# Kernel optimization log

Hardware: AMD Instinct MI355X
Metric: run time of the kernel (lower is better)

Reference implementation:

```python
import jax, jax.numpy as jnp
import numpy as np

T = 2048   # sequence length
K = 8      # anchor stride
B = 8      # batch
E = 64     # head dim


def make_coords(t, k):
    # Faithful vectorized version of get_coords2: for each anchor c in
    # {0, k, 2k, ...}, emit pairs (y, c) for y in [c, t).
    cs = np.arange(t // k) * k
    rows = np.concatenate([np.arange(c, t) for c in cs]).astype(np.int32)
    cols = np.concatenate([np.full(t - c, c, dtype=np.int32) for c in cs])
    return rows, cols


def setup_inputs() -> dict:
    key = jax.random.key(0)
    k1, k2, k3 = jax.random.split(key, 3)
    rows, cols = make_coords(T, K)  # np = 263168 nonzeros
    return {
        "k": jax.random.normal(k1, (B, T, E), dtype=jnp.float32),
        "q": jax.random.normal(k2, (B, T, E), dtype=jnp.float32),
        "v": jax.random.normal(k3, (B, T, E), dtype=jnp.float32),
        "rows": jnp.asarray(rows),
        "cols": jnp.asarray(cols),
    }


def reference(k, q, v, rows, cols):
    # dot[b, p] = <k[b, rows[p], :], q[b, cols[p], :]>  (calc_vals on k @ q^T)
    # out[b, y, :] = sum_{p: rows[p]==y} dot[b, p] * v[b, cols[p], :]
    #   (sparse.batchmm: sparse (t x t) matrix with values dot, times v)
    t = k.shape[1]

    def single(kb, qb, vb):
        dots = jnp.einsum("pe,pe->p", kb[rows], qb[cols])           # [np]
        contrib = dots[:, None] * vb[cols]                           # [np, e]
        return jax.ops.segment_sum(contrib, rows, num_segments=t)   # [t, e]

    return jax.vmap(single)(k, q, v)
```

## Files before the change

kernel.cpp:

```cpp
#include <hip/hip_runtime.h>
#include <hip/hip_bf16.h>


constexpr int T_LEN = 2048;
constexpr int EDIM  = 64;
constexpr int ROWS  = 32;
constexpr int NTILE = T_LEN / ROWS;
constexpr int TE    = T_LEN * EDIM;

typedef __attribute__((ext_vector_type(4))) float f32x4;
typedef __attribute__((ext_vector_type(8))) short bf16x8;

__device__ __forceinline__ short f2bf(float f) {
    __hip_bfloat16 h = __float2bfloat16(f);
    return __builtin_bit_cast(short, h);
}

__device__ __forceinline__ bf16x8 pack8(f32x4 a, f32x4 b) {
    bf16x8 r;
    r[0] = f2bf(a[0]); r[1] = f2bf(a[1]); r[2] = f2bf(a[2]); r[3] = f2bf(a[3]);
    r[4] = f2bf(b[0]); r[5] = f2bf(b[1]); r[6] = f2bf(b[2]); r[7] = f2bf(b[3]);
    return r;
}

__device__ __forceinline__ bf16x8 pack8a(const float* v) {
    bf16x8 r;
    #pragma unroll
    for (int i = 0; i < 8; ++i) r[i] = f2bf(v[i]);
    return r;
}

__device__ __forceinline__ void run_tile(const float* __restrict__ kb,
                                         const float* __restrict__ qb,
                                         const float* __restrict__ vb,
                                         int y0, int wpar, int lane,
                                         short* sl, f32x4 (&acc)[2][4])
{
    const int g  = lane >> 4;
    const int ln = lane & 15;

    bf16x8 Kf[2][2];
    #pragma unroll
    for (int mt = 0; mt < 2; ++mt)
        #pragma unroll
        for (int eh = 0; eh < 2; ++eh) {
            const float* p = kb + (size_t)(y0 + mt * 16 + ln) * EDIM + eh * 32 + g * 8;
            Kf[mt][eh] = pack8(*(const f32x4*)p, *(const f32x4*)(p + 4));
        }

    const int amax = (y0 + ROWS - 1) >> 3;
    const int nat  = (amax >> 5) + 1;

    for (int ai = wpar; ai < nat; ai += 2) {
        const int a0 = ai * 32;

        f32x4 qraw[2][2][2];
        #pragma unroll
        for (int nt = 0; nt < 2; ++nt)
            #pragma unroll
            for (int eh = 0; eh < 2; ++eh) {
                const float* p = qb + (size_t)(8 * (a0 + nt * 16 + ln)) * EDIM + eh * 32 + g * 8;
                qraw[nt][eh][0] = *(const f32x4*)p;
                qraw[nt][eh][1] = *(const f32x4*)(p + 4);
            }

        float vraw[4][8];
        {
            const float* pv = vb + (size_t)(8 * (a0 + 8 * g)) * EDIM + ln;
            #pragma unroll
            for (int i = 0; i < 8; ++i)
                #pragma unroll
                for (int et = 0; et < 4; ++et)
                    vraw[et][i] = pv[(size_t)i * 8 * EDIM + et * 16];
        }

        bf16x8 Qf[2][2];
        #pragma unroll
        for (int nt = 0; nt < 2; ++nt)
            #pragma unroll
            for (int eh = 0; eh < 2; ++eh)
                Qf[nt][eh] = pack8(qraw[nt][eh][0], qraw[nt][eh][1]);

        f32x4 S[2][2];
        #pragma unroll
        for (int mt = 0; mt < 2; ++mt)
            #pragma unroll
            for (int nt = 0; nt < 2; ++nt) {
                f32x4 s = {0.f, 0.f, 0.f, 0.f};
                s = __builtin_amdgcn_mfma_f32_16x16x32_bf16(Kf[mt][0], Qf[nt][0], s, 0, 0, 0);
                s = __builtin_amdgcn_mfma_f32_16x16x32_bf16(Kf[mt][1], Qf[nt][1], s, 0, 0, 0);
                S[mt][nt] = s;
            }

        if (ai == nat - 1) {
            #pragma unroll
            for (int mt = 0; mt < 2; ++mt)
                #pragma unroll
                for (int nt = 0; nt < 2; ++nt)
                    #pragma unroll
                    for (int r = 0; r < 4; ++r) {
                        int y = y0 + mt * 16 + g * 4 + r;
                        int a = a0 + nt * 16 + ln;
                        if (8 * a > y) S[mt][nt][r] = 0.f;
                    }
        }

        #pragma unroll
        for (int mt = 0; mt < 2; ++mt)
            #pragma unroll
            for (int nt = 0; nt < 2; ++nt)
                #pragma unroll
                for (int r = 0; r < 4; ++r) {
                    int row = mt * 16 + g * 4 + r;
                    int a   = nt * 16 + ln;
                    sl[row * 32 + (((a >> 3) ^ (row & 3)) << 3) + (a & 7)] = f2bf(S[mt][nt][r]);
                }

        bf16x8 SA[2];
        #pragma unroll
        for (int mt = 0; mt < 2; ++mt) {
            int row = mt * 16 + ln;
            SA[mt] = *(const bf16x8*)(sl + row * 32 + ((g ^ (row & 3)) << 3));
        }

        #pragma unroll
        for (int et = 0; et < 4; ++et) {
            bf16x8 Vf = pack8a(vraw[et]);
            #pragma unroll
            for (int mt = 0; mt < 2; ++mt)
                acc[mt][et] = __builtin_amdgcn_mfma_f32_16x16x32_bf16(SA[mt], Vf, acc[mt][et], 0, 0, 0);
        }
    }
}

__device__ __forceinline__ void write_partial(float (*pb)[EDIM], f32x4 (&acc)[2][4],
                                              int g, int ln)
{
    #pragma unroll
    for (int mt = 0; mt < 2; ++mt)
        #pragma unroll
        for (int et = 0; et < 4; ++et)
            #pragma unroll
            for (int r = 0; r < 4; ++r) {
                int row = mt * 16 + g * 4 + r;
                int e   = et * 16 + ln;
                pb[row][e ^ ((row & 3) << 2)] = acc[mt][et][r];
            }
}

__device__ __forceinline__ void store_add(float* o, float (*pb)[EDIM],
                                          f32x4 (&acc)[2][4], int g, int ln)
{
    #pragma unroll
    for (int mt = 0; mt < 2; ++mt)
        #pragma unroll
        for (int et = 0; et < 4; ++et)
            #pragma unroll
            for (int r = 0; r < 4; ++r) {
                int row = mt * 16 + g * 4 + r;
                int e   = et * 16 + ln;
                o[(size_t)row * EDIM + e] = acc[mt][et][r] + pb[row][e ^ ((row & 3) << 2)];
            }
}

__global__ __launch_bounds__(128, 1)
void sh2_mfma(const float* __restrict__ kk, const float* __restrict__ qq,
              const float* __restrict__ vv, float* __restrict__ out, int B)
{
    __shared__ alignas(16) short slds[2][ROWS * 32];
    __shared__ float pbuf[2][ROWS][EDIM];

    const int bid  = blockIdx.x;
    const int p    = bid & 31;
    const int b    = bid >> 5;
    const int w    = threadIdx.x >> 6;
    const int lane = threadIdx.x & 63;
    const int g = lane >> 4, ln = lane & 15;

    const float* kb = kk + (size_t)b * TE;
    const float* qb = qq + (size_t)b * TE;
    const float* vb = vv + (size_t)b * TE;

    const int y0A = ROWS * p;
    const int y0B = ROWS * (NTILE - 1 - p);

    const f32x4 vzero = {0.f, 0.f, 0.f, 0.f};
    f32x4 accA[2][4], accB[2][4];
    #pragma unroll
    for (int i = 0; i < 2; ++i)
        #pragma unroll
        for (int j = 0; j < 4; ++j) { accA[i][j] = vzero; accB[i][j] = vzero; }

    run_tile(kb, qb, vb, y0A, w, lane, slds[w], accA);
    if (w == 1) write_partial(pbuf[0], accA, g, ln);

    run_tile(kb, qb, vb, y0B, w, lane, slds[w], accB);
    if (w == 0) write_partial(pbuf[1], accB, g, ln);

    __syncthreads();

    if (w == 0) store_add(out + (size_t)b * TE + (size_t)y0A * EDIM, pbuf[0], accA, g, ln);
    else        store_add(out + (size_t)b * TE + (size_t)y0B * EDIM, pbuf[1], accB, g, ln);
}

extern "C" void kernel_launch(void* const* d_in, const int* in_sizes, int n_in,
                              void* d_out, int out_size, void* d_ws, size_t ws_size,
                              hipStream_t stream) {
    const float* kk = (const float*)d_in[0];
    const float* qq = (const float*)d_in[1];
    const float* vv = (const float*)d_in[2];
    float* o        = (float*)d_out;
    int B = in_sizes[0] / TE;
    sh2_mfma<<<B * (NTILE / 2), 128, 0, stream>>>(kk, qq, vv, o, B);
}
```

Baseline: 12.41 us.

## Precompute bf16 K, anchor Q and transposed V in a prep kernel

Adds a prep kernel that converts K to bf16, gathers the anchor rows of Q into a compact bf16 array, and writes V anchors transposed in bf16 to the workspace. The main kernel then loads MFMA operands directly as bf16x8 vectors instead of doing strided fp32 loads and per-element conversion. Work is redistributed to one 32-row tile per block with four waves splitting the anchor loop, reduced through padded shared memory. This costs a second launch and an extra global round trip through the workspace, and removes the tile pairing that balanced the triangular work per block.

```diff
diff --git a/kernel.cpp b/kernel.cpp
--- a/kernel.cpp
+++ b/kernel.cpp
@@ -4,89 +4,116 @@
 
 constexpr int T_LEN = 2048;
 constexpr int EDIM  = 64;
+constexpr int NA    = 256;
 constexpr int ROWS  = 32;
 constexpr int NTILE = T_LEN / ROWS;
 constexpr int TE    = T_LEN * EDIM;
+constexpr int AE    = NA * EDIM;
 
 typedef __attribute__((ext_vector_type(4))) float f32x4;
 typedef __attribute__((ext_vector_type(8))) short bf16x8;
+typedef __attribute__((ext_vector_type(4))) short bf16x4;
 
 __device__ __forceinline__ short f2bf(float f) {
     __hip_bfloat16 h = __float2bfloat16(f);
     return __builtin_bit_cast(short, h);
 }
 
-__device__ __forceinline__ bf16x8 pack8(f32x4 a, f32x4 b) {
-    bf16x8 r;
-    r[0] = f2bf(a[0]); r[1] = f2bf(a[1]); r[2] = f2bf(a[2]); r[3] = f2bf(a[3]);
-    r[4] = f2bf(b[0]); r[5] = f2bf(b[1]); r[6] = f2bf(b[2]); r[7] = f2bf(b[3]);
-    return r;
+__global__ __launch_bounds__(256)
+void sh2_prep(const float* __restrict__ kk, const float* __restrict__ qq,
+              const float* __restrict__ vv, short* __restrict__ ws, int B)
+{
+    const int nK = B * TE / 4;
+    const int nQ = B * AE / 4;
+    short* Qa = ws;
+    short* Vt = ws + (size_t)B * AE;
+    short* Kb = ws + (size_t)2 * B * AE;
+
+    int tid = blockIdx.x * 256 + threadIdx.x;
+    if (tid < nK) {
+        f32x4 x = *(const f32x4*)(kk + (size_t)tid * 4);
+        bf16x4 r;
+        #pragma unroll
+        for (int i = 0; i < 4; ++i) r[i] = f2bf(x[i]);
+        *(bf16x4*)(Kb + (size_t)tid * 4) = r;
+    } else if (tid < nK + nQ) {
+        int t = tid - nK;
+        int e4 = t & 15, a = (t >> 4) & 255, b = t >> 12;
+        f32x4 x = *(const f32x4*)(qq + ((size_t)b * T_LEN + 8 * a) * EDIM + e4 * 4);
+        bf16x4 r;
+        #pragma unroll
+        for (int i = 0; i < 4; ++i) r[i] = f2bf(x[i]);
+        *(bf16x4*)(Qa + (size_t)t * 4) = r;
+    } else if (tid < nK + 2 * nQ) {
+        int t = tid - nK - nQ;
+        int a4 = t & 63, e = (t >> 6) & 63, b = t >> 12;
+        bf16x4 r;
+        #pragma unroll
+        for (int i = 0; i < 4; ++i)
+            r[i] = f2bf(vv[((size_t)b * T_LEN + 8 * (a4 * 4 + i)) * EDIM + e]);
+        *(bf16x4*)(Vt + (size_t)t * 4) = r;
+    }
 }
 
-__device__ __forceinline__ bf16x8 pack8a(const float* v) {
-    bf16x8 r;
-    #pragma unroll
-    for (int i = 0; i < 8; ++i) r[i] = f2bf(v[i]);
-    return r;
-}
+constexpr int EP = 76;
 
-__device__ __forceinline__ void run_tile(const float* __restrict__ kb,
-                                         const float* __restrict__ qb,
-                                         const float* __restrict__ vb,
-                                         int y0, int wpar, int lane,
-                                         short* sl, f32x4 (&acc)[2][4])
+__global__ __launch_bounds__(256, 2)
+void sh2_main(const short* __restrict__ ws, float* __restrict__ out, int B)
 {
-    const int g  = lane >> 4;
-    const int ln = lane & 15;
+    __shared__ alignas(16) short slds[4][ROWS * 32];
+    __shared__ float pbuf[4][ROWS][EP];
+
+    const int bid = blockIdx.x;
+    const int p   = NTILE - 1 - (bid >> 3);
+    const int b   = bid & 7;
+    const int w    = threadIdx.x >> 6;
+    const int lane = threadIdx.x & 63;
+    const int g = lane >> 4, ln = lane & 15;
+
+    const short* Qa = ws + (size_t)b * AE;
+    const short* Vt = ws + (size_t)B * AE + (size_t)b * AE;
+    const short* Kb = ws + (size_t)2 * B * AE + (size_t)b * TE;
+
+    const int y0  = ROWS * p;
+    const int nat = (((4 * p + 3) >> 5)) + 1;
 
     bf16x8 Kf[2][2];
     #pragma unroll
     for (int mt = 0; mt < 2; ++mt)
         #pragma unroll
-        for (int eh = 0; eh < 2; ++eh) {
-            const float* p = kb + (size_t)(y0 + mt * 16 + ln) * EDIM + eh * 32 + g * 8;
-            Kf[mt][eh] = pack8(*(const f32x4*)p, *(const f32x4*)(p + 4));
-        }
+        for (int eh = 0; eh < 2; ++eh)
+            Kf[mt][eh] = *(const bf16x8*)(Kb + (size_t)(y0 + mt * 16 + ln) * EDIM + eh * 32 + g * 8);
 
-    const int amax = (y0 + ROWS - 1) >> 3;
-    const int nat  = (amax >> 5) + 1;
+    const f32x4 vzero = {0.f, 0.f, 0.f, 0.f};
+    f32x4 acc[2][4];
+    #pragma unroll
+    for (int i = 0; i < 2; ++i)
+        #pragma unroll
+        for (int j = 0; j < 4; ++j) acc[i][j] = vzero;
 
-    for (int ai = wpar; ai < nat; ai += 2) {
+    short* sl = slds[w];
+
+    for (int ai = w; ai < nat; ai += 4) {
         const int a0 = ai * 32;
-
-        f32x4 qraw[2][2][2];
-        #pragma unroll
-        for (int nt = 0; nt < 2; ++nt)
-            #pragma unroll
-            for (int eh = 0; eh < 2; ++eh) {
-                const float* p = qb + (size_t)(8 * (a0 + nt * 16 + ln)) * EDIM + eh * 32 + g * 8;
-                qraw[nt][eh][0] = *(const f32x4*)p;
-                qraw[nt][eh][1] = *(const f32x4*)(p + 4);
-            }
-
-        float vraw[4][8];
-        {
-            const float* pv = vb + (size_t)(8 * (a0 + 8 * g)) * EDIM + ln;
-            #pragma unroll
-            for (int i = 0; i < 8; ++i)
-                #pragma unroll
-                for (int et = 0; et < 4; ++et)
-                    vraw[et][i] = pv[(size_t)i * 8 * EDIM + et * 16];
-        }
 
         bf16x8 Qf[2][2];
         #pragma unroll
         for (int nt = 0; nt < 2; ++nt)
             #pragma unroll
             for (int eh = 0; eh < 2; ++eh)
-                Qf[nt][eh] = pack8(qraw[nt][eh][0], qraw[nt][eh][1]);
+                Qf[nt][eh] = *(const bf16x8*)(Qa + (size_t)(a0 + nt * 16 + ln) * EDIM + eh * 32 + g * 8);
+
+        bf16x8 Vf[4];
+        #pragma unroll
+        for (int et = 0; et < 4; ++et)
+            Vf[et] = *(const bf16x8*)(Vt + (size_t)(et * 16 + ln) * NA + a0 + g * 8);
 
         f32x4 S[2][2];
         #pragma unroll
         for (int mt = 0; mt < 2; ++mt)
             #pragma unroll
             for (int nt = 0; nt < 2; ++nt) {
-                f32x4 s = {0.f, 0.f, 0.f, 0.f};
+                f32x4 s = vzero;
                 s = __builtin_amdgcn_mfma_f32_16x16x32_bf16(Kf[mt][0], Qf[nt][0], s, 0, 0, 0);
                 s = __builtin_amdgcn_mfma_f32_16x16x32_bf16(Kf[mt][1], Qf[nt][1], s, 0, 0, 0);
                 S[mt][nt] = s;
@@ -113,94 +140,44 @@
                 for (int r = 0; r < 4; ++r) {
                     int row = mt * 16 + g * 4 + r;
                     int a   = nt * 16 + ln;
-                    sl[row * 32 + (((a >> 3) ^ (row & 3)) << 3) + (a & 7)] = f2bf(S[mt][nt][r]);
+                    sl[row * 32 + ((((a >> 3) ^ ((row >> 2) & 3))) << 3) + (a & 7)] = f2bf(S[mt][nt][r]);
                 }
 
         bf16x8 SA[2];
         #pragma unroll
         for (int mt = 0; mt < 2; ++mt) {
             int row = mt * 16 + ln;
-            SA[mt] = *(const bf16x8*)(sl + row * 32 + ((g ^ (row & 3)) << 3));
+            SA[mt] = *(const bf16x8*)(sl + row * 32 + ((g ^ ((row >> 2) & 3)) << 3));
         }
 
         #pragma unroll
-        for (int et = 0; et < 4; ++et) {
-            bf16x8 Vf = pack8a(vraw[et]);
+        for (int et = 0; et < 4; ++et)
             #pragma unroll
             for (int mt = 0; mt < 2; ++mt)
-                acc[mt][et] = __builtin_amdgcn_mfma_f32_16x16x32_bf16(SA[mt], Vf, acc[mt][et], 0, 0, 0);
-        }
+                acc[mt][et] = __builtin_amdgcn_mfma_f32_16x16x32_bf16(SA[mt], Vf[et], acc[mt][et], 0, 0, 0);
     }
-}
 
-__device__ __forceinline__ void write_partial(float (*pb)[EDIM], f32x4 (&acc)[2][4],
-                                              int g, int ln)
-{
     #pragma unroll
     for (int mt = 0; mt < 2; ++mt)
         #pragma unroll
         for (int et = 0; et < 4; ++et)
             #pragma unroll
-            for (int r = 0; r < 4; ++r) {
-                int row = mt * 16 + g * 4 + r;
-                int e   = et * 16 + ln;
-                pb[row][e ^ ((row & 3) << 2)] = acc[mt][et][r];
-            }
-}
-
-__device__ __forceinline__ void store_add(float* o, float (*pb)[EDIM],
-                                          f32x4 (&acc)[2][4], int g, int ln)
-{
-    #pragma unroll
-    for (int mt = 0; mt < 2; ++mt)
-        #pragma unroll
-        for (int et = 0; et < 4; ++et)
-            #pragma unroll
-            for (int r = 0; r < 4; ++r) {
-                int row = mt * 16 + g * 4 + r;
-                int e   = et * 16 + ln;
-                o[(size_t)row * EDIM + e] = acc[mt][et][r] + pb[row][e ^ ((row & 3) << 2)];
-            }
-}
-
-__global__ __launch_bounds__(128, 1)
-void sh2_mfma(const float* __restrict__ kk, const float* __restrict__ qq,
-              const float* __restrict__ vv, float* __restrict__ out, int B)
-{
-    __shared__ alignas(16) short slds[2][ROWS * 32];
-    __shared__ float pbuf[2][ROWS][EDIM];
-
-    const int bid  = blockIdx.x;
-    const int p    = bid & 31;
-    const int b    = bid >> 5;
-    const int w    = threadIdx.x >> 6;
-    const int lane = threadIdx.x & 63;
-    const int g = lane >> 4, ln = lane & 15;
-
-    const float* kb = kk + (size_t)b * TE;
-    const float* qb = qq + (size_t)b * TE;
-    const float* vb = vv + (size_t)b * TE;
-
-    const int y0A = ROWS * p;
-    const int y0B = ROWS * (NTILE - 1 - p);
-
-    const f32x4 vzero = {0.f, 0.f, 0.f, 0.f};
-    f32x4 accA[2][4], accB[2][4];
-    #pragma unroll
-    for (int i = 0; i < 2; ++i)
-        #pragma unroll
-        for (int j = 0; j < 4; ++j) { accA[i][j] = vzero; accB[i][j] = vzero; }
-
-    run_tile(kb, qb, vb, y0A, w, lane, slds[w], accA);
-    if (w == 1) write_partial(pbuf[0], accA, g, ln);
-
-    run_tile(kb, qb, vb, y0B, w, lane, slds[w], accB);
-    if (w == 0) write_partial(pbuf[1], accB, g, ln);
+            for (int r = 0; r < 4; ++r)
+                pbuf[w][mt * 16 + g * 4 + r][et * 16 + ln] = acc[mt][et][r];
 
     __syncthreads();
 
-    if (w == 0) store_add(out + (size_t)b * TE + (size_t)y0A * EDIM, pbuf[0], accA, g, ln);
-    else        store_add(out + (size_t)b * TE + (size_t)y0B * EDIM, pbuf[1], accB, g, ln);
+    const int row = w * 8 + (lane >> 3);
+    const int e0  = (lane & 7) * 8;
+    f32x4 s0 = vzero, s1 = vzero;
+    #pragma unroll
+    for (int w2 = 0; w2 < 4; ++w2) {
+        s0 += *(const f32x4*)&pbuf[w2][row][e0];
+        s1 += *(const f32x4*)&pbuf[w2][row][e0 + 4];
+    }
+    float* o = out + ((size_t)b * T_LEN + y0 + row) * EDIM + e0;
+    *(f32x4*)o       = s0;
+    *(f32x4*)(o + 4) = s1;
 }
 
 extern "C" void kernel_launch(void* const* d_in, const int* in_sizes, int n_in,
@@ -210,6 +187,11 @@
     const float* qq = (const float*)d_in[1];
     const float* vv = (const float*)d_in[2];
     float* o        = (float*)d_out;
+    short* ws       = (short*)d_ws;
     int B = in_sizes[0] / TE;
-    sh2_mfma<<<B * (NTILE / 2), 128, 0, stream>>>(kk, qq, vv, o, B);
+
+    int prep_units = B * TE / 4 + 2 * (B * AE / 4);
+    int prep_grid  = (prep_units + 255) / 256;
+    sh2_prep<<<prep_grid, 256, 0, stream>>>(kk, qq, vv, ws, B);
+    sh2_main<<<B * NTILE, 256, 0, stream>>>(ws, o, B);
 }
```

Measured after the change: 15.80 us. +27.3%, slower.
